# Kernel optimization log

Hardware: AMD Instinct MI355X
Metric: run time of the kernel (lower is better)

The kernel has to match this reference:

```python
import jax, jax.numpy as jnp
import numpy as np

N = 50000      # nodes
E = 800000     # edges (avg degree 16)
IN = 128       # in_feats
OUT = 128      # out_feats
ASSIGN = 256   # assign_dim = B graphs * 8 clusters
B = 32         # batch_size (num graphs)


def setup_inputs() -> dict:
    key = jax.random.key(0)
    k0, k1, k2, k3 = jax.random.split(key, 4)
    x = jax.random.normal(k0, (N, IN), jnp.float32)
    edge_index = jax.random.randint(k1, (2, E), 0, N, dtype=jnp.int32)
    # sorted graph ids, ~equal-sized graphs (mirrors block_diag mask construction)
    batch = ((jnp.arange(N, dtype=jnp.int32) * B) // N).astype(jnp.int32)
    # SAGEConv params: Linear(2*in_feats -> out) on concat([x, mean_neigh])
    W_embed = jax.random.normal(k2, (2 * IN, OUT), jnp.float32) / np.float32(np.sqrt(2 * IN))
    b_embed = jnp.zeros((OUT,), jnp.float32)
    W_pool = jax.random.normal(k3, (2 * IN, ASSIGN), jnp.float32) / np.float32(np.sqrt(2 * IN))
    b_pool = jnp.zeros((ASSIGN,), jnp.float32)
    return dict(x=x, edge_index=edge_index, batch=batch,
                W_embed=W_embed, b_embed=b_embed, W_pool=W_pool, b_pool=b_pool)


def _sage(x, src, dst, W, b):
    # mean aggregation over in-neighbors (messages src -> dst), then Linear on concat
    n = x.shape[0]
    deg = jax.ops.segment_sum(jnp.ones((src.shape[0],), x.dtype), dst, num_segments=n)
    neigh = jax.ops.segment_sum(x[src], dst, num_segments=n) / jnp.maximum(deg, 1.0)[:, None]
    return jnp.concatenate([x, neigh], axis=-1) @ W + b


def reference(x, edge_index, batch, W_embed, b_embed, W_pool, b_pool):
    src, dst = edge_index[0], edge_index[1]
    embed = _sage(x, src, dst, W_embed, b_embed)                      # [N, OUT]
    pooled = jax.nn.softmax(_sage(x, src, dst, W_pool, b_pool), -1)   # [N, ASSIGN]
    # block-diagonal mask: node i of graph g sees columns [g*C, (g+1)*C)
    C = ASSIGN // B
    cols = jnp.arange(ASSIGN, dtype=batch.dtype) // C
    mask = (batch[:, None] == cols[None, :]).astype(x.dtype)          # [N, ASSIGN]
    # NOTE: faithful to original: softmax of (mask * pooled), zeros contribute exp(0)
    r = jax.nn.softmax(mask * pooled, axis=-1) * mask
    r = r / (r.sum(axis=-1, keepdims=True) + 1e-13)                   # [N, ASSIGN]
    h = r.T @ embed                                                   # [ASSIGN, OUT]
    # adj_new = S^T A S with A sparse COO (rows=edge_index[0], cols=edge_index[1])
    ar = jax.ops.segment_sum(r[dst], src, num_segments=x.shape[0])    # A @ S : [N, ASSIGN]
    adj_new = r.T @ ar                                                # [ASSIGN, ASSIGN]
    return (adj_new, h)
```

## Files before the change

### kernel.cpp

```cpp
#include <hip/hip_runtime.h>
#include <hip/hip_bf16.h>

#define N_ 50000
#define E_ 800000
#define IN_ 128
#define OUT_ 128
#define ASSIGN_ 256
#define B_ 32
#define KTOT 256
#define JTOT 384
#define HCHUNK 32
#define ACHUNK 32
#define AST 72
#define NXP ((N_ + 127) / 128)
#define NGB (NXP * 3)
#define NCVX 6250

#define NBKT 128
#define NPB 391
#define BCAP 7000
#define EPB 4096
#define NBLK_A ((E_ + EPB - 1) / EPB)
#define NPRE (NBLK_A + NCVX + 384)

typedef __attribute__((ext_vector_type(8))) short short8;
typedef __attribute__((ext_vector_type(4))) float f32x4;
typedef __attribute__((ext_vector_type(2))) float f32x2;
typedef __attribute__((ext_vector_type(4))) unsigned short ushort4v;
typedef __attribute__((ext_vector_type(2))) unsigned short ushort2v;
typedef unsigned short u16;

__device__ inline unsigned short f2bf(float v) {
    union { float f; unsigned u; } a;
    a.f = v;
    unsigned r = a.u + 0x7fff + ((a.u >> 16) & 1);
    return (unsigned short)(r >> 16);
}
__device__ inline float bf2f(unsigned short b) {
    union { unsigned u; float f; } a;
    a.u = ((unsigned)b) << 16;
    return a.f;
}

__device__ inline unsigned enc8(float v) {
    union { float f; unsigned u; } a;
    a.f = v * 0x1p-120f;
    unsigned b = a.u;
    unsigned r = b + 0x7FFFF + ((b >> 20) & 1);
    return ((r >> 20) & 0x7F) | ((b >> 24) & 0x80);
}
__device__ inline float2 dec8x2(unsigned short p) {
#if defined(__has_builtin) && __has_builtin(__builtin_amdgcn_cvt_pk_f32_fp8)
    f32x2 r = __builtin_amdgcn_cvt_pk_f32_fp8((int)(unsigned)p, false);
    return make_float2(r.x, r.y);
#else
    unsigned u0 = p & 0xffu, u1 = (p >> 8) & 0xffu;
    union { unsigned u; float f; } a, b;
    a.u = ((u0 & 0x80u) << 24) | ((u0 & 0x7fu) << 20);
    b.u = ((u1 & 0x80u) << 24) | ((u1 & 0x7fu) << 20);
    return make_float2(a.f * 0x1p+120f, b.f * 0x1p+120f);
#endif
}

__global__ __launch_bounds__(256) void k_pre(const int* __restrict__ ei,
                                             int* __restrict__ bktFill,
                                             int2* __restrict__ ebkt,
                                             const float* __restrict__ x,
                                             unsigned short* __restrict__ xhi,
                                             unsigned char* __restrict__ xq,
                                             const float* __restrict__ We,
                                             const float* __restrict__ be,
                                             const float* __restrict__ Wp,
                                             const float* __restrict__ bp,
                                             unsigned short* __restrict__ WThi,
                                             float* __restrict__ bias) {
    __shared__ int lh[NBKT], lbase[NBKT], lofs[NBKT];
    int bid = blockIdx.x;
    int t = threadIdx.x;
    if (bid < NBLK_A) {
        int e0 = bid * EPB;
        if (t < NBKT) { lh[t] = 0; lofs[t] = 0; }
        __syncthreads();
        int ss[16], dd[16];
#pragma unroll
        for (int i = 0; i < 16; i++) {
            int e = e0 + i * 256 + t;
            ss[i] = 0; dd[i] = -1;
            if (e < E_) {
                ss[i] = ei[e];
                dd[i] = ei[E_ + e];
                atomicAdd(&lh[dd[i] / NPB], 1);
            }
        }
        __syncthreads();
        if (t < NBKT) lbase[t] = t * BCAP + atomicAdd(&bktFill[t], lh[t]);
        __syncthreads();
#pragma unroll
        for (int i = 0; i < 16; i++) {
            if (dd[i] >= 0) {
                int b = dd[i] / NPB;
                int o = atomicAdd(&lofs[b], 1);
                ebkt[lbase[b] + o] = make_int2(ss[i], dd[i]);
            }
        }
        return;
    }
    if (bid >= NBLK_A + NCVX) {
        int idx = (bid - NBLK_A - NCVX) * 256 + t;
        if (idx < JTOT * KTOT) {
            int j = idx / KTOT, k = idx - j * KTOT;
            float v = (j < 128) ? We[k * 128 + j] : Wp[k * 256 + (j - 128)];
            WThi[idx] = f2bf(v);
        }
        if (idx < JTOT) bias[idx] = (idx < 128) ? be[idx] : bp[idx - 128];
        return;
    }
    int i4 = ((bid - NBLK_A) * 256 + t) * 4;
    if (i4 >= N_ * 128) return;
    float4 v = *(const float4*)(x + i4);
    ushort4v h;
    h.x = f2bf(v.x); h.y = f2bf(v.y); h.z = f2bf(v.z); h.w = f2bf(v.w);
    *(ushort4v*)(xhi + i4) = h;
    unsigned q = enc8(v.x) | (enc8(v.y) << 8) | (enc8(v.z) << 16) | (enc8(v.w) << 24);
    *(unsigned*)(xq + i4) = q;
}

__global__ __launch_bounds__(256) void k_binB0(const int* __restrict__ bktFill,
                                               const int2* __restrict__ ebkt,
                                               int* __restrict__ locOff,
                                               int* __restrict__ bucketTotal) {
    __shared__ int ldeg[NPB];
    __shared__ int lscan[512];
    int b = blockIdx.x, t = threadIdx.x;
    for (int i = t; i < NPB; i += 256) ldeg[i] = 0;
    __syncthreads();
    int base = b * BCAP;
    int cnt = bktFill[b];
    int n0 = b * NPB;
    for (int j = t; j < cnt; j += 256)
        atomicAdd(&ldeg[ebkt[base + j].y - n0], 1);
    __syncthreads();
    lscan[t] = (t < NPB) ? ldeg[t] : 0;
    lscan[t + 256] = (t + 256 < NPB) ? ldeg[t + 256] : 0;
    __syncthreads();
    for (int off = 1; off < 512; off <<= 1) {
        int x0 = lscan[t];
        int x1 = lscan[t + 256];
        int a0 = (t >= off) ? lscan[t - off] : 0;
        int a1 = (t + 256 >= off) ? lscan[t + 256 - off] : 0;
        __syncthreads();
        lscan[t] = x0 + a0;
        lscan[t + 256] = x1 + a1;
        __syncthreads();
    }
    for (int i = t; i < NPB; i += 256) {
        int n = n0 + i;
        if (n < N_) locOff[n] = (i == 0) ? 0 : lscan[i - 1];
    }
    if (t == 0) bucketTotal[b] = lscan[NPB - 1];
}

__global__ __launch_bounds__(256) void k_binB1(const int* __restrict__ bktFill,
                                               const int2* __restrict__ ebkt,
                                               const int* __restrict__ locOff,
                                               const int* __restrict__ bucketTotal,
                                               int* __restrict__ rowStart,
                                               int* __restrict__ csr_src,
                                               int* __restrict__ csr_dst) {
    __shared__ int lfill[NPB];
    __shared__ int bsc[NBKT];
    int b = blockIdx.x, t = threadIdx.x;
    if (t < NBKT) bsc[t] = bucketTotal[t];
    __syncthreads();
    for (int off = 1; off < NBKT; off <<= 1) {
        int x = (t < NBKT) ? bsc[t] : 0;
        int add = (t < NBKT && t >= off) ? bsc[t - off] : 0;
        __syncthreads();
        if (t < NBKT) bsc[t] = x + add;
        __syncthreads();
    }
    int base0 = (b == 0) ? 0 : bsc[b - 1];
    int n0 = b * NPB;
    for (int i = t; i < NPB; i += 256) {
        int n = n0 + i;
        if (n < N_) {
            int lo = locOff[n];
            lfill[i] = lo;
            rowStart[n] = base0 + lo;
        }
    }
    __syncthreads();
    int base = b * BCAP;
    int cnt = bktFill[b];
    for (int j = t; j < cnt; j += 256) {
        int2 sd = ebkt[base + j];
        int p = base0 + atomicAdd(&lfill[sd.y - n0], 1);
        csr_src[p] = sd.x;
        csr_dst[p] = sd.y;
    }
    if (b == 0 && t == 0) rowStart[N_] = E_;
}

__global__ __launch_bounds__(256) void k_agg(const unsigned char* __restrict__ xq,
                                             const int* __restrict__ rowStart,
                                             const int* __restrict__ csr_src,
                                             unsigned short* __restrict__ nhi) {
    int node = blockIdx.x * 4 + (threadIdx.x >> 6);
    if (node >= N_) return;
    int lane = threadIdx.x & 63;
    int l5 = lane & 31;
    int eh = lane >> 5;
    int a = rowStart[node], bnd = rowStart[node + 1];
    float a0 = 0.f, a1 = 0.f, a2 = 0.f, a3 = 0.f;
    int j = a;
    for (; j + 7 < bnd; j += 8) {
        unsigned q[4];
#pragma unroll
        for (int ii = 0; ii < 4; ii++) {
            int s = csr_src[j + 2 * ii + eh];
            q[ii] = *(const unsigned*)(xq + (size_t)s * 128 + l5 * 4);
        }
#pragma unroll
        for (int ii = 0; ii < 4; ii++) {
            float2 f01 = dec8x2((unsigned short)(q[ii] & 0xffffu));
            float2 f23 = dec8x2((unsigned short)(q[ii] >> 16));
            a0 += f01.x; a1 += f01.y; a2 += f23.x; a3 += f23.y;
        }
    }
    for (; j < bnd; j += 2) {
        unsigned qq = 0;
        int e = j + eh;
        if (e < bnd) {
            int s = csr_src[e];
            qq = *(const unsigned*)(xq + (size_t)s * 128 + l5 * 4);
        }
        float2 f01 = dec8x2((unsigned short)(qq & 0xffffu));
        float2 f23 = dec8x2((unsigned short)(qq >> 16));
        a0 += f01.x; a1 += f01.y; a2 += f23.x; a3 += f23.y;
    }
    a0 += __shfl_xor(a0, 32, 64);
    a1 += __shfl_xor(a1, 32, 64);
    a2 += __shfl_xor(a2, 32, 64);
    a3 += __shfl_xor(a3, 32, 64);
    float inv = 1.0f / (float)max(bnd - a, 1);
    if (lane < 32) {
        ushort4v h;
        h.x = f2bf(a0 * inv);
        h.y = f2bf(a1 * inv);
        h.z = f2bf(a2 * inv);
        h.w = f2bf(a3 * inv);
        *(ushort4v*)(nhi + (size_t)node * 128 + l5 * 4) = h;
    }
}

#define LDA 40
__global__ __launch_bounds__(256) void k_gemm(const unsigned short* __restrict__ xhi,
                                              const unsigned short* __restrict__ nhi,
                                              const unsigned short* __restrict__ WThi,
                                              const float* __restrict__ bias,
                                              unsigned short* __restrict__ embed,
                                              unsigned short* __restrict__ plog) {
    __shared__ __align__(16) union {
        struct { u16 Ah[128][LDA]; u16 Bh[128][LDA]; } s;
        u16 ep[64 * 128];
    } sm;
    int t = threadIdx.x;
    int wave = t >> 6, lane = t & 63;
    int wm = wave >> 1, wn = wave & 1;
    int q = lane >> 4, lr = lane & 15;

    int id = blockIdx.x;
    int xi, cc;
    if (id < (NXP / 8) * 24) {
        xi = (id / 24) * 8 + (id & 7);
        cc = (id % 24) >> 3;
    } else {
        int r2 = id - (NXP / 8) * 24;
        xi = (NXP / 8) * 8 + r2 % (NXP % 8);
        cc = r2 / (NXP % 8);
    }
    int row0 = xi * 128;
    int col0 = cc * 128;

    f32x4 acc[4][4] = {};
    int smr = t >> 1;
    int kc = (t & 1) * 16;

    for (int kt = 0; kt < KTOT; kt += 32) {
        const u16* Ah_src = (kt < 128) ? xhi : nhi;
        int kb = (kt & 127) + kc;
        int node = row0 + smr;
        short8 vh0 = {}, vh1 = {};
        if (node < N_) {
            const short8* ph = (const short8*)(Ah_src + (size_t)node * 128 + kb);
            vh0 = ph[0]; vh1 = ph[1];
        }
        *(short8*)&sm.s.Ah[smr][kc] = vh0;
        *(short8*)&sm.s.Ah[smr][kc + 8] = vh1;
        {
            const short8* ph = (const short8*)(WThi + (size_t)(col0 + smr) * 256 + kt + kc);
            short8 wh0 = ph[0], wh1 = ph[1];
            *(short8*)&sm.s.Bh[smr][kc] = wh0;
            *(short8*)&sm.s.Bh[smr][kc + 8] = wh1;
        }
        __syncthreads();

        short8 afh[4];
#pragma unroll
        for (int mi = 0; mi < 4; mi++) {
            int r = wm * 64 + mi * 16 + lr;
            afh[mi] = *(const short8*)&sm.s.Ah[r][q * 8];
        }
#pragma unroll
        for (int ni = 0; ni < 4; ni++) {
            int r = wn * 64 + ni * 16 + lr;
            short8 bfh = *(const short8*)&sm.s.Bh[r][q * 8];
#pragma unroll
            for (int mi = 0; mi < 4; mi++)
                acc[mi][ni] = __builtin_amdgcn_mfma_f32_16x16x32_bf16(afh[mi], bfh, acc[mi][ni], 0, 0, 0);
        }
        __syncthreads();
    }

    for (int half = 0; half < 2; half++) {
        __syncthreads();
        if (wm == half) {
#pragma unroll
            for (int mi = 0; mi < 4; mi++)
#pragma unroll
                for (int ni = 0; ni < 4; ni++) {
                    int lcol = wn * 64 + ni * 16 + lr;
                    float bj = bias[col0 + lcol];
#pragma unroll
                    for (int r = 0; r < 4; r++) {
                        int lrow = mi * 16 + q * 4 + r;
                        sm.ep[lrow * 128 + lcol] = f2bf(acc[mi][ni][r] + bj);
                    }
                }
        }
        __syncthreads();
#pragma unroll
        for (int i = 0; i < 4; i++) {
            int chunk = i * 256 + t;
            int lrow = chunk >> 4;
            int lco = (chunk & 15) * 8;
            int grow = row0 + half * 64 + lrow;
            if (grow < N_) {
                short8 v = *(const short8*)&sm.ep[lrow * 128 + lco];
                if (col0 < 128)
                    *(short8*)(embed + (size_t)grow * 128 + lco) = v;
                else
                    *(short8*)(plog + (size_t)grow * 256 + (col0 - 128) + lco) = v;
            }
        }
    }
}

__global__ __launch_bounds__(256) void k_r(const unsigned short* __restrict__ plog,
                                           const int* __restrict__ batch,
                                           float* __restrict__ r8,
                                           unsigned short* __restrict__ r8b) {
    int node = blockIdx.x * 4 + (threadIdx.x >> 6);
    int lane = threadIdx.x & 63;
    if (node >= N_) return;
    ushort4v p4 = *(const ushort4v*)(plog + (size_t)node * 256 + lane * 4);
    float px = bf2f(p4.x), py = bf2f(p4.y), pz = bf2f(p4.z), pw = bf2f(p4.w);
    float m = fmaxf(fmaxf(px, py), fmaxf(pz, pw));
    for (int off = 32; off; off >>= 1) m = fmaxf(m, __shfl_xor(m, off, 64));
    float s = expf(px - m) + expf(py - m) + expf(pz - m) + expf(pw - m);
    for (int off = 32; off; off >>= 1) s += __shfl_xor(s, off, 64);
    int g = batch[node];
    float v = 0.f;
    if (lane < 8) v = expf(bf2f(plog[(size_t)node * 256 + g * 8 + lane]) - m) / s;
    float M2 = v;
    for (int off = 4; off; off >>= 1) M2 = fmaxf(M2, __shfl_xor(M2, off, 64));
    float e = expf(v - M2);
    float Sg = e;
    for (int off = 4; off; off >>= 1) Sg += __shfl_xor(Sg, off, 64);
    float D2 = Sg + 248.0f * expf(-M2);
    float r = e / (Sg + 1e-13f * D2);
    if (lane < 8) {
        r8[node * 8 + lane] = r;
        r8b[node * 8 + lane] = f2bf(r);
    }
}

__global__ __launch_bounds__(256) void k_tail(const int* __restrict__ rowStart,
                                              const int* __restrict__ csr_src,
                                              const int* __restrict__ csr_dst,
                                              const unsigned short* __restrict__ r8b,
                                              float* __restrict__ partAdj,
                                              const unsigned short* __restrict__ embed,
                                              const float* __restrict__ r8,
                                              float* __restrict__ partH) {
    __shared__ __align__(16) unsigned short Ab[256 * AST];
    __shared__ __align__(16) unsigned short Bb[16 * AST];
    int id = blockIdx.x;
    int t = threadIdx.x;
    if (id >= B_ * ACHUNK) {
        int idh = id - B_ * ACHUNK;
        int g = idh & 31;
        int c = idh >> 5;
        int o = t & 127, half = t >> 7;
        int n0g = (g * N_ + 31) >> 5;
        int n1g = ((g + 1) * N_ + 31) >> 5;
        int len = n1g - n0g;
        int a = n0g + (len * c) / HCHUNK;
        int b = n0g + (len * (c + 1)) / HCHUNK;
        float a0 = 0.f, a1 = 0.f, a2 = 0.f, a3 = 0.f;
#pragma unroll 4
        for (int n = a; n < b; n++) {
            float e = bf2f(embed[(size_t)n * 128 + o]);
            const float* rr = r8 + n * 8 + half;
            a0 += rr[0] * e;
            a1 += rr[2] * e;
            a2 += rr[4] * e;
            a3 += rr[6] * e;
        }
        float* pb = partH + (g * HCHUNK + c) * 1024;
        pb[(half + 0) * 128 + o] = a0;
        pb[(half + 2) * 128 + o] = a1;
        pb[(half + 4) * 128 + o] = a2;
        pb[(half + 6) * 128 + o] = a3;
        return;
    }
    int gd = id & 31;
    int c = id >> 5;
    int wave = t >> 6, lane = t & 63;
    int q = lane >> 4, lr = lane & 15;
    int n0g = (gd * N_ + 31) >> 5;
    int n1g = ((gd + 1) * N_ + 31) >> 5;
    int len = n1g - n0g;
    int na = n0g + (len * c) / ACHUNK;
    int nb = n0g + (len * (c + 1)) / ACHUNK;
    int j0 = rowStart[na], j1 = rowStart[nb];

    uint4 z = {0, 0, 0, 0};
#pragma unroll
    for (int i = 0; i < 9; i++) *(uint4*)&Ab[(i * 256 + t) * 8] = z;
    if (t < 144) *(uint4*)&Bb[t * 8] = z;
    __syncthreads();

    f32x4 acc[4] = {};
    int el = t >> 2;
    int ap = t & 3;

    for (int jt = j0; jt < j1; jt += 64) {
        int j = jt + el;
        int ca = -1;
        if (j < j1) {
            int s = csr_src[j];
            int d = csr_dst[j];
            int gs = (s * B_) / N_;
            unsigned sv = *(const unsigned*)(r8b + (size_t)s * 8 + ap * 2);
            unsigned dv = *(const unsigned*)(r8b + (size_t)d * 8 + ap * 2);
            ca = gs * 8 + ap * 2;
            Ab[ca * AST + el] = (unsigned short)sv;
            Ab[(ca + 1) * AST + el] = (unsigned short)(sv >> 16);
            Bb[(ap * 2) * AST + el] = (unsigned short)dv;
            Bb[(ap * 2 + 1) * AST + el] = (unsigned short)(dv >> 16);
        }
        __syncthreads();
        short8 bf0 = *(const short8*)&Bb[lr * AST + q * 8];
        short8 bf1 = *(const short8*)&Bb[lr * AST + 32 + q * 8];
#pragma unroll
        for (int mi = 0; mi < 4; mi++) {
            int col = (wave * 4 + mi) * 16 + lr;
            short8 a0 = *(const short8*)&Ab[col * AST + q * 8];
            short8 a1 = *(const short8*)&Ab[col * AST + 32 + q * 8];
            acc[mi] = __builtin_amdgcn_mfma_f32_16x16x32_bf16(a0, bf0, acc[mi], 0, 0, 0);
            acc[mi] = __builtin_amdgcn_mfma_f32_16x16x32_bf16(a1, bf1, acc[mi], 0, 0, 0);
        }
        __syncthreads();
        if (ca >= 0) {
            Ab[ca * AST + el] = 0;
            Ab[(ca + 1) * AST + el] = 0;
            Bb[(ap * 2) * AST + el] = 0;
            Bb[(ap * 2 + 1) * AST + el] = 0;
        }
        __syncthreads();
    }

    float* pb = partAdj + (gd * ACHUNK + c) * 2048;
    if (lr < 8) {
#pragma unroll
        for (int mi = 0; mi < 4; mi++) {
            int mbase = (wave * 4 + mi) * 16 + q * 4;
#pragma unroll
            for (int r = 0; r < 4; r++)
                pb[(mbase + r) * 8 + lr] = acc[mi][r];
        }
    }
}

__global__ __launch_bounds__(256) void k_red(const float* __restrict__ partAdj,
                                             const float* __restrict__ partH,
                                             float* __restrict__ out) {
    int o = blockIdx.x * 256 + threadIdx.x;
    if (o < 256 * 256) {
        int row = o >> 8, col = o & 255;
        int gd = col >> 3, b = col & 7;
        int li = row * 8 + b;
        float s = 0.f;
#pragma unroll
        for (int c = 0; c < ACHUNK; c++) s += partAdj[(gd * ACHUNK + c) * 2048 + li];
        out[o] = s;
    } else {
        int idx = o - 256 * 256;
        int g = idx >> 10;
        int local = idx & 1023;
        float s = 0.f;
#pragma unroll
        for (int c = 0; c < HCHUNK; c++) s += partH[(g * HCHUNK + c) * 1024 + local];
        out[256 * 256 + idx] = s;
    }
}

extern "C" void kernel_launch(void* const* d_in, const int* in_sizes, int n_in,
                              void* d_out, int out_size, void* d_ws, size_t ws_size,
                              hipStream_t stream) {
    const float* x = (const float*)d_in[0];
    const int* ei = (const int*)d_in[1];
    const int* batch = (const int*)d_in[2];
    const float* We = (const float*)d_in[3];
    const float* be = (const float*)d_in[4];
    const float* Wp = (const float*)d_in[5];
    const float* bp = (const float*)d_in[6];
    float* out = (float*)d_out;

    char* w = (char*)d_ws;
    auto alloc = [&](size_t bytes) -> char* {
        char* p = w;
        w += (bytes + 255) & ~(size_t)255;
        return p;
    };
    unsigned short* xhi = (unsigned short*)alloc((size_t)N_ * 128 * 2);
    unsigned char* xq = (unsigned char*)alloc((size_t)N_ * 128);
    unsigned short* nhi = (unsigned short*)alloc((size_t)N_ * 128 * 2);
    unsigned short* WThi = (unsigned short*)alloc((size_t)JTOT * KTOT * 2);
    unsigned short* embed = (unsigned short*)alloc((size_t)N_ * 128 * 2);
    unsigned short* plog = (unsigned short*)alloc((size_t)N_ * 256 * 2);
    float* r8 = (float*)alloc((size_t)N_ * 8 * 4);
    unsigned short* r8b = (unsigned short*)alloc((size_t)N_ * 8 * 2);
    float* bias = (float*)alloc(JTOT * 4);
    int* locOff = (int*)alloc((size_t)N_ * 4);
    int* rowStart = (int*)alloc((size_t)(N_ + 1) * 4);
    int* csr_src = (int*)alloc((size_t)E_ * 4);
    int* csr_dst = (int*)alloc((size_t)E_ * 4);
    int* bucketTotal = (int*)alloc(NBKT * 4);
    int* bktFill = (int*)alloc(NBKT * 4);
    int2* ebkt = (int2*)alloc((size_t)NBKT * BCAP * 8);
    float* partH = (float*)alloc((size_t)B_ * HCHUNK * 1024 * 4);
    float* partAdj = (float*)alloc((size_t)B_ * ACHUNK * 2048 * 4);

    hipMemsetAsync(bktFill, 0, NBKT * 4, stream);
    k_pre<<<NPRE, 256, 0, stream>>>(ei, bktFill, ebkt, x, xhi, xq, We, be, Wp, bp, WThi, bias);
    k_binB0<<<NBKT, 256, 0, stream>>>(bktFill, ebkt, locOff, bucketTotal);
    k_binB1<<<NBKT, 256, 0, stream>>>(bktFill, ebkt, locOff, bucketTotal, rowStart, csr_src, csr_dst);
    k_agg<<<(N_ + 3) / 4, 256, 0, stream>>>(xq, rowStart, csr_src, nhi);
    k_gemm<<<NGB, 256, 0, stream>>>(xhi, nhi, WThi, bias, embed, plog);
    k_r<<<(N_ + 3) / 4, 256, 0, stream>>>(plog, batch, r8, r8b);
    k_tail<<<2 * B_ * ACHUNK, 256, 0, stream>>>(rowStart, csr_src, csr_dst, r8b, partAdj, embed, r8, partH);
    k_red<<<(256 * 256 + 256 * 128 + 255) / 256, 256, 0, stream>>>(partAdj, partH, out);
}
```

Measured before the change: 228.5 us.

## Fuse CSR binning kernels via inter-block flag sync and prefetch GEMM tiles

Merges the two CSR binning kernels into one. Each block publishes its bucket total through a global ready flag and spin-waits on the flags of all 128 buckets, which removes a kernel launch and the locOff round trip through global memory. This relies on all 128 blocks being resident at the same time. The GEMM main loop also register-prefetches the next K-slice of A and B before the MFMA work, overlapping global loads with compute at the cost of extra registers.

```diff
diff --git a/kernel.cpp b/kernel.cpp
--- a/kernel.cpp
+++ b/kernel.cpp
@@ -125,12 +125,16 @@
     *(unsigned*)(xq + i4) = q;
 }
 
-__global__ __launch_bounds__(256) void k_binB0(const int* __restrict__ bktFill,
-                                               const int2* __restrict__ ebkt,
-                                               int* __restrict__ locOff,
-                                               int* __restrict__ bucketTotal) {
+__global__ __launch_bounds__(256) void k_binB(const int* __restrict__ bktFill,
+                                              const int2* __restrict__ ebkt,
+                                              int* __restrict__ ready,
+                                              int* __restrict__ rowStart,
+                                              int* __restrict__ csr_src,
+                                              int* __restrict__ csr_dst) {
     __shared__ int ldeg[NPB];
     __shared__ int lscan[512];
+    __shared__ int bsc[NBKT];
+    __shared__ int lfill[NPB];
     int b = blockIdx.x, t = threadIdx.x;
     for (int i = t; i < NPB; i += 256) ldeg[i] = 0;
     __syncthreads();
@@ -153,24 +157,12 @@
         lscan[t + 256] = x1 + a1;
         __syncthreads();
     }
-    for (int i = t; i < NPB; i += 256) {
-        int n = n0 + i;
-        if (n < N_) locOff[n] = (i == 0) ? 0 : lscan[i - 1];
-    }
-    if (t == 0) bucketTotal[b] = lscan[NPB - 1];
-}
-
-__global__ __launch_bounds__(256) void k_binB1(const int* __restrict__ bktFill,
-                                               const int2* __restrict__ ebkt,
-                                               const int* __restrict__ locOff,
-                                               const int* __restrict__ bucketTotal,
-                                               int* __restrict__ rowStart,
-                                               int* __restrict__ csr_src,
-                                               int* __restrict__ csr_dst) {
-    __shared__ int lfill[NPB];
-    __shared__ int bsc[NBKT];
-    int b = blockIdx.x, t = threadIdx.x;
-    if (t < NBKT) bsc[t] = bucketTotal[t];
+    if (t == 0) atomicExch(&ready[b], lscan[NPB - 1] + 1);
+    if (t < NBKT) {
+        int v;
+        while ((v = atomicAdd(&ready[t], 0)) == 0) __builtin_amdgcn_s_sleep(8);
+        bsc[t] = v - 1;
+    }
     __syncthreads();
     for (int off = 1; off < NBKT; off <<= 1) {
         int x = (t < NBKT) ? bsc[t] : 0;
@@ -180,18 +172,15 @@
         __syncthreads();
     }
     int base0 = (b == 0) ? 0 : bsc[b - 1];
-    int n0 = b * NPB;
     for (int i = t; i < NPB; i += 256) {
         int n = n0 + i;
         if (n < N_) {
-            int lo = locOff[n];
-            lfill[i] = lo;
-            rowStart[n] = base0 + lo;
+            int excl = (i == 0) ? 0 : lscan[i - 1];
+            lfill[i] = excl;
+            rowStart[n] = base0 + excl;
         }
     }
     __syncthreads();
-    int base = b * BCAP;
-    int cnt = bktFill[b];
     for (int j = t; j < cnt; j += 256) {
         int2 sd = ebkt[base + j];
         int p = base0 + atomicAdd(&lfill[sd.y - n0], 1);
@@ -285,25 +274,29 @@
     f32x4 acc[4][4] = {};
     int smr = t >> 1;
     int kc = (t & 1) * 16;
-
+    int node = row0 + smr;
+
+    short8 vh0, vh1, wh0, wh1;
+#define LOADK(KT)                                                                    \
+    {                                                                                \
+        const u16* Ah_src = ((KT) < 128) ? xhi : nhi;                                \
+        int kb = ((KT) & 127) + kc;                                                  \
+        vh0 = {}; vh1 = {};                                                          \
+        if (node < N_) {                                                             \
+            const short8* ph = (const short8*)(Ah_src + (size_t)node * 128 + kb);    \
+            vh0 = ph[0]; vh1 = ph[1];                                                \
+        }                                                                            \
+        const short8* pw = (const short8*)(WThi + (size_t)(col0 + smr) * 256 + (KT) + kc); \
+        wh0 = pw[0]; wh1 = pw[1];                                                    \
+    }
+    LOADK(0);
     for (int kt = 0; kt < KTOT; kt += 32) {
-        const u16* Ah_src = (kt < 128) ? xhi : nhi;
-        int kb = (kt & 127) + kc;
-        int node = row0 + smr;
-        short8 vh0 = {}, vh1 = {};
-        if (node < N_) {
-            const short8* ph = (const short8*)(Ah_src + (size_t)node * 128 + kb);
-            vh0 = ph[0]; vh1 = ph[1];
-        }
         *(short8*)&sm.s.Ah[smr][kc] = vh0;
         *(short8*)&sm.s.Ah[smr][kc + 8] = vh1;
-        {
-            const short8* ph = (const short8*)(WThi + (size_t)(col0 + smr) * 256 + kt + kc);
-            short8 wh0 = ph[0], wh1 = ph[1];
-            *(short8*)&sm.s.Bh[smr][kc] = wh0;
-            *(short8*)&sm.s.Bh[smr][kc + 8] = wh1;
-        }
-        __syncthreads();
+        *(short8*)&sm.s.Bh[smr][kc] = wh0;
+        *(short8*)&sm.s.Bh[smr][kc + 8] = wh1;
+        __syncthreads();
+        if (kt + 32 < KTOT) LOADK(kt + 32);
 
         short8 afh[4];
 #pragma unroll
@@ -321,6 +314,7 @@
         }
         __syncthreads();
     }
+#undef LOADK
 
     for (int half = 0; half < 2; half++) {
         __syncthreads();
@@ -543,20 +537,18 @@
     float* r8 = (float*)alloc((size_t)N_ * 8 * 4);
     unsigned short* r8b = (unsigned short*)alloc((size_t)N_ * 8 * 2);
     float* bias = (float*)alloc(JTOT * 4);
-    int* locOff = (int*)alloc((size_t)N_ * 4);
     int* rowStart = (int*)alloc((size_t)(N_ + 1) * 4);
     int* csr_src = (int*)alloc((size_t)E_ * 4);
     int* csr_dst = (int*)alloc((size_t)E_ * 4);
-    int* bucketTotal = (int*)alloc(NBKT * 4);
-    int* bktFill = (int*)alloc(NBKT * 4);
+    int* bktFill = (int*)alloc(2 * NBKT * 4);
+    int* ready = bktFill + NBKT;
     int2* ebkt = (int2*)alloc((size_t)NBKT * BCAP * 8);
     float* partH = (float*)alloc((size_t)B_ * HCHUNK * 1024 * 4);
     float* partAdj = (float*)alloc((size_t)B_ * ACHUNK * 2048 * 4);
 
-    hipMemsetAsync(bktFill, 0, NBKT * 4, stream);
+    hipMemsetAsync(bktFill, 0, 2 * NBKT * 4, stream);
     k_pre<<<NPRE, 256, 0, stream>>>(ei, bktFill, ebkt, x, xhi, xq, We, be, Wp, bp, WThi, bias);
-    k_binB0<<<NBKT, 256, 0, stream>>>(bktFill, ebkt, locOff, bucketTotal);
-    k_binB1<<<NBKT, 256, 0, stream>>>(bktFill, ebkt, locOff, bucketTotal, rowStart, csr_src, csr_dst);
+    k_binB<<<NBKT, 256, 0, stream>>>(bktFill, ebkt, ready, rowStart, csr_src, csr_dst);
     k_agg<<<(N_ + 3) / 4, 256, 0, stream>>>(xq, rowStart, csr_src, nhi);
     k_gemm<<<NGB, 256, 0, stream>>>(xhi, nhi, WThi, bias, embed, plog);
     k_r<<<(N_ + 3) / 4, 256, 0, stream>>>(plog, batch, r8, r8b);
```

Result: no change. 224.2 us (-1.9%).
